# Kernel optimization log

Measured on AMD Instinct MI355X. Metric: run time of the kernel, lower is better.

## Reference

```python
import jax, jax.numpy as jnp
import numpy as np

N, E, B = 100000, 3200000, 1024
D_LM, K, H, C, L = 1024, 128, 256, 40, 2
T = 0.1
LN_EPS = 1e-5


def _layernorm(x, g, b):
    m = x.mean(-1, keepdims=True)
    v = ((x - m) ** 2).mean(-1, keepdims=True)
    return (x - m) * jax.lax.rsqrt(v + LN_EPS) * g + b


def _gcn_conv(x, W, b, src, dst, norm, self_w):
    h = x @ W
    agg = jax.ops.segment_sum(h[src] * norm[:, None], dst, num_segments=N)
    return agg + h * self_w[:, None] + b


def setup_inputs() -> dict:
    key = jax.random.key(0)
    ks = jax.random.split(key, 20)
    s = 0.02
    rn = lambda k, shp: jax.random.normal(k, shp, jnp.float32) * s
    return {
        "hidden_embeds": jax.random.normal(ks[0], (L, N, D_LM), jnp.float32),
        "proj_W1": rn(ks[1], (L, D_LM, K)),
        "proj_b1": jnp.zeros((L, K), jnp.float32),
        "ln_g": jnp.ones((L, K), jnp.float32),
        "ln_b": jnp.zeros((L, K), jnp.float32),
        "proj_W2": rn(ks[2], (L, K, K)),
        "proj_b2": jnp.zeros((L, K), jnp.float32),
        "alphas": jnp.zeros((L,), jnp.float32),
        "gcn_W1": rn(ks[3], (L, K, H)),
        "gcn_b1": jnp.zeros((L, H), jnp.float32),
        "gcn_W2": rn(ks[4], (L, H, K)),
        "gcn_b2": jnp.zeros((L, K), jnp.float32),
        "clf_W": rn(ks[5], (2 * K, C)),
        "clf_b": jnp.zeros((C,), jnp.float32),
        "edge_index": jax.random.randint(ks[6], (2, E), 0, N, jnp.int64 if jax.config.jax_enable_x64 else jnp.int32),
        "mapping": jax.random.randint(ks[7], (B,), 0, N, jnp.int64 if jax.config.jax_enable_x64 else jnp.int32),
    }


def reference(hidden_embeds, proj_W1, proj_b1, ln_g, ln_b, proj_W2, proj_b2,
              alphas, gcn_W1, gcn_b1, gcn_W2, gcn_b2, clf_W, clf_b,
              edge_index, mapping):
    src, dst = edge_index[0], edge_index[1]
    ones = jnp.ones((E,), jnp.float32)
    # GCN normalization (self loops included): deg over dst + 1
    deg = jax.ops.segment_sum(ones, dst, num_segments=N) + 1.0
    dis = jax.lax.rsqrt(deg)
    norm = dis[src] * dis[dst]          # per-edge D^-1/2 A D^-1/2
    self_w = 1.0 / deg                  # self-loop weight dis[i]*dis[i]

    last = None
    for i in range(L):
        # projector: Linear -> LayerNorm -> ReLU -> Linear
        h = hidden_embeds[i] @ proj_W1[i] + proj_b1[i]
        h = jax.nn.relu(_layernorm(h, ln_g[i], ln_b[i]))
        h = h @ proj_W2[i] + proj_b2[i]
        if i > 0:
            a = jax.nn.sigmoid(alphas[i] / T)
            h = h * a + last * (1.0 - a)
        # 2-layer GCN encoder (dropout=0)
        z = jax.nn.relu(_gcn_conv(h, gcn_W1[i], gcn_b1[i], src, dst, norm, self_w))
        last = _gcn_conv(z, gcn_W2[i], gcn_b2[i], src, dst, norm, self_w)

    # custom_global_mean_pool: mean over {node} U {out-neighbors} U {in-neighbors}
    sum_n = (jax.ops.segment_sum(last[dst], src, num_segments=N)
             + jax.ops.segment_sum(last[src], dst, num_segments=N))
    cnt = (jax.ops.segment_sum(ones, src, num_segments=N)
           + jax.ops.segment_sum(ones, dst, num_segments=N))
    pooled = (last[mapping] + sum_n[mapping]) / (1.0 + cnt[mapping])[:, None]

    out = jnp.concatenate([last[mapping], pooled], axis=1)  # [B, 2K]
    return out @ clf_W + clf_b
```

## Files before the change

kernel.cpp:

```cpp
#include <hip/hip_runtime.h>
#include <hip/hip_bf16.h>
#include <math.h>

using short8 = __attribute__((ext_vector_type(8))) short;
using f32x4  = __attribute__((ext_vector_type(4))) float;

#define PSTRIDE 2048

__device__ __forceinline__ short f2bf(float f) {
    __hip_bfloat16 h = __float2bfloat16(f);
    return *reinterpret_cast<short*>(&h);
}


__global__ void map_scatter_k(const int* __restrict__ mapping, int* __restrict__ map_idx, int B)
{
    int b = blockIdx.x * blockDim.x + threadIdx.x;
    if (b < B) map_idx[mapping[b]] = b;
}

__launch_bounds__(1024)
__global__ void bin_count_k(const int* __restrict__ dst, int E, int* __restrict__ bin_cnt)
{
    __shared__ int h[4096];
    for (int i = threadIdx.x; i < 4096; i += 1024) h[i] = 0;
    __syncthreads();
    int base = blockIdx.x * 32768;
#pragma unroll
    for (int i = 0; i < 32; ++i) {
        int e = base + i * 1024 + threadIdx.x;
        if (e < E) atomicAdd(&h[dst[e] >> 5], 1);
    }
    __syncthreads();
    for (int i = threadIdx.x; i < 4096; i += 1024) {
        int c = h[i];
        if (c) atomicAdd(&bin_cnt[i], c);
    }
}

__launch_bounds__(1024)
__global__ void scan_bins_k(const int* __restrict__ cnt, int* __restrict__ off,
                            int* __restrict__ cur)
{
    __shared__ int wsum[16];
    int tid = threadIdx.x, lane = tid & 63, wid = tid >> 6;
    int4 v = ((const int4*)cnt)[tid];
    int s0 = v.x, s1 = s0 + v.y, s2 = s1 + v.z, s3 = s2 + v.w;
    int q = s3;
#pragma unroll
    for (int o = 1; o < 64; o <<= 1) { int t = __shfl_up(q, o); if (lane >= o) q += t; }
    if (lane == 63) wsum[wid] = q;
    __syncthreads();
    if (wid == 0) {
        int w = (lane < 16) ? wsum[lane] : 0;
#pragma unroll
        for (int o = 1; o < 16; o <<= 1) { int t = __shfl_up(w, o); if (lane >= o) w += t; }
        if (lane < 16) wsum[lane] = w;
    }
    __syncthreads();
    int base = (wid ? wsum[wid - 1] : 0) + q - s3;
    int4 o4; o4.x = base; o4.y = base + s0; o4.z = base + s1; o4.w = base + s2;
    ((int4*)off)[tid] = o4;
    ((int4*)cur)[tid] = o4;
    if (tid == 1023) off[4096] = base + s3;
}

__launch_bounds__(256)
__global__ void bin_scatter_k(const int* __restrict__ ei, int E,
                              const int* __restrict__ map_idx,
                              int* __restrict__ bin_cur, int2* __restrict__ pairs,
                              int* __restrict__ pcnt, int* __restrict__ pnb)
{
    int e = blockIdx.x * blockDim.x + threadIdx.x;
    if (e >= E) return;
    int s = ei[e];
    int d = ei[E + e];
    int p = atomicAdd(&bin_cur[d >> 5], 1);
    pairs[p] = make_int2(s, d);
    int ms = map_idx[s];
    if (ms >= 0) {
        int i = atomicAdd(&pcnt[ms], 1);
        if (i < PSTRIDE) pnb[ms * PSTRIDE + i] = d;
    }
    int md = map_idx[d];
    if (md >= 0) {
        int i = atomicAdd(&pcnt[md], 1);
        if (i < PSTRIDE) pnb[md * PSTRIDE + i] = s;
    }
}

__launch_bounds__(256)
__global__ void bin_csr_k(const int2* __restrict__ pairs, const int* __restrict__ bin_off,
                          int* __restrict__ csr_in, int* __restrict__ in_off,
                          float* __restrict__ dis, float* __restrict__ selfw, int N)
{
    __shared__ int lcnt[32];
    __shared__ int lofs[32];
    __shared__ int lcur[32];
    int b = blockIdx.x;
    int tid = threadIdx.x;
    if (tid < 32) lcnt[tid] = 0;
    __syncthreads();
    int beg = bin_off[b], end = bin_off[b + 1];
    for (int i = beg + tid; i < end; i += 256)
        atomicAdd(&lcnt[pairs[i].y & 31], 1);
    __syncthreads();
    if (tid == 0) {
        int run = beg;
#pragma unroll
        for (int j = 0; j < 32; ++j) { lofs[j] = run; lcur[j] = run; run += lcnt[j]; }
    }
    __syncthreads();
    int n0 = b * 32;
    if (tid < 32 && n0 + tid < N) {
        in_off[n0 + tid] = lofs[tid];
        float dg = (float)lcnt[tid] + 1.0f;
        dis[n0 + tid] = rsqrtf(dg);
        selfw[n0 + tid] = 1.0f / dg;
    }
    if (b == gridDim.x - 1 && tid == 0) in_off[N] = end;
    for (int i = beg + tid; i < end; i += 256) {
        int2 pr = pairs[i];
        int p = atomicAdd(&lcur[pr.y & 31], 1);
        csr_in[p] = pr.x;
    }
}

__global__ void transpose_w_k(const float* __restrict__ src, short* __restrict__ dst,
                              int R, int Cc)
{
    int idx = blockIdx.x * blockDim.x + threadIdx.x;
    if (idx >= R * Cc) return;
    int r = idx / Cc;
    int c = idx - r * Cc;
    dst[(size_t)c * R + r] = f2bf(src[idx]);
}

__launch_bounds__(256)
__global__ void proj_fused_k(const float* __restrict__ X,
                             const short* __restrict__ W1t,
                             const float* __restrict__ b1,
                             const float* __restrict__ lng,
                             const float* __restrict__ lnb,
                             const short* __restrict__ W2t,
                             const float* __restrict__ b2,
                             const float* __restrict__ alphas, int layer,
                             const float* __restrict__ last,
                             short* __restrict__ out, int nrows)
{
    __shared__ short S[26624];

    const int tid  = threadIdx.x;
    const int lane = tid & 63;
    const int wave = tid >> 6;
    const int wr   = wave >> 1;
    const int wc   = wave & 1;
    const int g    = lane >> 4;
    const int lr   = lane & 15;
    const int row0 = blockIdx.x * 128;

    f32x4 acc[4][4];
#pragma unroll
    for (int fr = 0; fr < 4; ++fr)
#pragma unroll
        for (int fc = 0; fc < 4; ++fc) acc[fr][fc] = (f32x4){0.f, 0.f, 0.f, 0.f};

    const int xr   = tid >> 1;
    const int xc0  = (tid & 1) * 32;
    const bool xvalid = (row0 + xr) < nrows;
    const float* xbase = X + (size_t)(row0 + xr) * 1024 + xc0;
    const short* wbase = W1t + (size_t)(tid >> 1) * 1024 + (tid & 1) * 32;

    float4 xv[8];
    short8 wv[4];
    if (xvalid) {
#pragma unroll
        for (int m = 0; m < 8; ++m) xv[m] = *(const float4*)&xbase[m * 4];
    } else {
#pragma unroll
        for (int m = 0; m < 8; ++m) xv[m] = make_float4(0.f, 0.f, 0.f, 0.f);
    }
#pragma unroll
    for (int m = 0; m < 4; ++m) wv[m] = *(const short8*)&wbase[m * 8];

    for (int k0 = 0; k0 < 1024; k0 += 64) {
#pragma unroll
        for (int m = 0; m < 4; ++m) {
            short8 p;
            p[0]=f2bf(xv[2*m].x); p[1]=f2bf(xv[2*m].y); p[2]=f2bf(xv[2*m].z); p[3]=f2bf(xv[2*m].w);
            p[4]=f2bf(xv[2*m+1].x); p[5]=f2bf(xv[2*m+1].y); p[6]=f2bf(xv[2*m+1].z); p[7]=f2bf(xv[2*m+1].w);
            *(short8*)&S[xr * 72 + xc0 + m * 8] = p;
        }
#pragma unroll
        for (int m = 0; m < 4; ++m)
            *(short8*)&S[9216 + (tid >> 1) * 72 + (tid & 1) * 32 + m * 8] = wv[m];
        __syncthreads();

        if (k0 + 64 < 1024) {
            if (xvalid) {
                const float* xp = xbase + k0 + 64;
#pragma unroll
                for (int m = 0; m < 8; ++m) xv[m] = *(const float4*)&xp[m * 4];
            }
            const short* wp = wbase + k0 + 64;
#pragma unroll
            for (int m = 0; m < 4; ++m) wv[m] = *(const short8*)&wp[m * 8];
        }

#pragma unroll
        for (int kk = 0; kk < 64; kk += 32) {
            short8 a[4], b[4];
#pragma unroll
            for (int fr = 0; fr < 4; ++fr)
                a[fr] = *(short8*)&S[(wr * 64 + fr * 16 + lr) * 72 + kk + g * 8];
#pragma unroll
            for (int fc = 0; fc < 4; ++fc)
                b[fc] = *(short8*)&S[9216 + (wc * 64 + fc * 16 + lr) * 72 + kk + g * 8];
#pragma unroll
            for (int fr = 0; fr < 4; ++fr)
#pragma unroll
                for (int fc = 0; fc < 4; ++fc)
                    acc[fr][fc] = __builtin_amdgcn_mfma_f32_16x16x32_bf16(a[fr], b[fc], acc[fr][fc], 0, 0, 0);
        }
        __syncthreads();
    }

    float* P = (float*)&S[17408];
    {
        float b1v[4], gv[4], bv[4];
#pragma unroll
        for (int fc = 0; fc < 4; ++fc) {
            int col = wc * 64 + fc * 16 + lr;
            b1v[fc] = b1[col]; gv[fc] = lng[col]; bv[fc] = lnb[col];
        }
#pragma unroll
        for (int fr = 0; fr < 4; ++fr) {
#pragma unroll
            for (int j = 0; j < 4; ++j) {
                float s = 0.f, q = 0.f;
#pragma unroll
                for (int fc = 0; fc < 4; ++fc) {
                    float t = acc[fr][fc][j] + b1v[fc];
                    acc[fr][fc][j] = t;
                    s += t; q += t * t;
                }
#pragma unroll
                for (int m = 1; m < 16; m <<= 1) {
                    s += __shfl_xor(s, m);
                    q += __shfl_xor(q, m);
                }
                if (lr == 0) {
                    int row = wr * 64 + fr * 16 + 4 * g + j;
                    P[row * 4 + wc * 2]     = s;
                    P[row * 4 + wc * 2 + 1] = q;
                }
            }
        }
        __syncthreads();
#pragma unroll
        for (int fr = 0; fr < 4; ++fr) {
#pragma unroll
            for (int j = 0; j < 4; ++j) {
                int row = wr * 64 + fr * 16 + 4 * g + j;
                float s = P[row * 4 + 0] + P[row * 4 + 2];
                float q = P[row * 4 + 1] + P[row * 4 + 3];
                float mean = s * (1.0f / 128.0f);
                float var  = q * (1.0f / 128.0f) - mean * mean;
                float inv  = rsqrtf(var + 1e-5f);
#pragma unroll
                for (int fc = 0; fc < 4; ++fc) {
                    float h = fmaxf((acc[fr][fc][j] - mean) * inv * gv[fc] + bv[fc], 0.f);
                    S[row * 136 + wc * 64 + fc * 16 + lr] = f2bf(h);
                }
            }
        }
    }
    __syncthreads();

    f32x4 acc2[4][4];
#pragma unroll
    for (int fr = 0; fr < 4; ++fr)
#pragma unroll
        for (int fc = 0; fc < 4; ++fc) acc2[fr][fc] = (f32x4){0.f, 0.f, 0.f, 0.f};

    for (int k0 = 0; k0 < 128; k0 += 64) {
        {
            int c  = tid >> 1;
            int kb = (tid & 1) * 32;
            const short* wp = W2t + (size_t)c * 128 + k0 + kb;
#pragma unroll
            for (int m = 0; m < 4; ++m)
                *(short8*)&S[17408 + c * 72 + kb + m * 8] = *(const short8*)&wp[m * 8];
        }
        __syncthreads();
#pragma unroll
        for (int kk = 0; kk < 64; kk += 32) {
            short8 a[4], b[4];
#pragma unroll
            for (int fr = 0; fr < 4; ++fr)
                a[fr] = *(short8*)&S[(wr * 64 + fr * 16 + lr) * 136 + k0 + kk + g * 8];
#pragma unroll
            for (int fc = 0; fc < 4; ++fc)
                b[fc] = *(short8*)&S[17408 + (wc * 64 + fc * 16 + lr) * 72 + kk + g * 8];
#pragma unroll
            for (int fr = 0; fr < 4; ++fr)
#pragma unroll
                for (int fc = 0; fc < 4; ++fc)
                    acc2[fr][fc] = __builtin_amdgcn_mfma_f32_16x16x32_bf16(a[fr], b[fc], acc2[fr][fc], 0, 0, 0);
        }
        __syncthreads();
    }

    float b2v[4];
#pragma unroll
    for (int fc = 0; fc < 4; ++fc) b2v[fc] = b2[wc * 64 + fc * 16 + lr];
    float asig = 0.f, omas = 0.f;
    if (last) {
        float al = alphas[layer];
        asig = 1.0f / (1.0f + expf(-al * 10.0f));
        omas = 1.0f - asig;
    }
#pragma unroll
    for (int fr = 0; fr < 4; ++fr) {
#pragma unroll
        for (int j = 0; j < 4; ++j) {
            int gr = row0 + wr * 64 + fr * 16 + 4 * g + j;
            if (gr >= nrows) continue;
#pragma unroll
            for (int fc = 0; fc < 4; ++fc) {
                int col = wc * 64 + fc * 16 + lr;
                float o = acc2[fr][fc][j] + b2v[fc];
                if (last) o = asig * o + omas * last[(size_t)gr * 128 + col];
                out[(size_t)gr * 128 + col] = f2bf(o);
            }
        }
    }
}

__launch_bounds__(256)
__global__ void gcn_mlp_k(const short* __restrict__ U,
                          const short* __restrict__ W1t,
                          const float* __restrict__ gb1,
                          const short* __restrict__ W2t,
                          short* __restrict__ V, int M)
{
    __shared__ short S[35840];

    const int tid  = threadIdx.x;
    const int lane = tid & 63;
    const int wave = tid >> 6;
    const int g    = lane >> 4;
    const int lr   = lane & 15;
    const int m0   = blockIdx.x * 64;

#pragma unroll
    for (int it = 0; it < 4; ++it) {
        int i = tid + it * 256;
        int r = i >> 4;
        int c8 = i & 15;
        short8 v = {0,0,0,0,0,0,0,0};
        int gr = m0 + r;
        if (gr < M) v = *(const short8*)&U[(size_t)gr * 128 + c8 * 8];
        *(short8*)&S[r * 136 + c8 * 8] = v;
    }

    f32x4 acc[4][4];
#pragma unroll
    for (int fr = 0; fr < 4; ++fr)
#pragma unroll
        for (int fc = 0; fc < 4; ++fc) acc[fr][fc] = (f32x4){0.f, 0.f, 0.f, 0.f};

    for (int k0 = 0; k0 < 128; k0 += 64) {
#pragma unroll
        for (int it = 0; it < 8; ++it) {
            int i = tid + it * 256;
            int r = i >> 3;
            int c8 = i & 7;
            *(short8*)&S[17408 + r * 72 + c8 * 8] =
                *(const short8*)&W1t[(size_t)r * 128 + k0 + c8 * 8];
        }
        __syncthreads();
#pragma unroll
        for (int kk = 0; kk < 64; kk += 32) {
            short8 a[4], b[4];
#pragma unroll
            for (int fr = 0; fr < 4; ++fr)
                a[fr] = *(short8*)&S[(fr * 16 + lr) * 136 + k0 + kk + g * 8];
#pragma unroll
            for (int fc = 0; fc < 4; ++fc)
                b[fc] = *(short8*)&S[17408 + (wave * 64 + fc * 16 + lr) * 72 + kk + g * 8];
#pragma unroll
            for (int fr = 0; fr < 4; ++fr)
#pragma unroll
                for (int fc = 0; fc < 4; ++fc)
                    acc[fr][fc] = __builtin_amdgcn_mfma_f32_16x16x32_bf16(a[fr], b[fc], acc[fr][fc], 0, 0, 0);
        }
        __syncthreads();
    }

    {
        float bb[4];
#pragma unroll
        for (int fc = 0; fc < 4; ++fc) bb[fc] = gb1[wave * 64 + fc * 16 + lr];
#pragma unroll
        for (int fr = 0; fr < 4; ++fr) {
#pragma unroll
            for (int j = 0; j < 4; ++j) {
                int rloc = fr * 16 + 4 * g + j;
#pragma unroll
                for (int fc = 0; fc < 4; ++fc) {
                    float zv = fmaxf(acc[fr][fc][j] + bb[fc], 0.f);
                    S[rloc * 264 + wave * 64 + fc * 16 + lr] = f2bf(zv);
                }
            }
        }
    }

    f32x4 acc2[4][2];
#pragma unroll
    for (int fr = 0; fr < 4; ++fr) {
        acc2[fr][0] = (f32x4){0.f, 0.f, 0.f, 0.f};
        acc2[fr][1] = (f32x4){0.f, 0.f, 0.f, 0.f};
    }

    for (int k0 = 0; k0 < 256; k0 += 64) {
#pragma unroll
        for (int it = 0; it < 4; ++it) {
            int i = tid + it * 256;
            int r = i >> 3;
            int c8 = i & 7;
            *(short8*)&S[16896 + r * 72 + c8 * 8] =
                *(const short8*)&W2t[(size_t)r * 256 + k0 + c8 * 8];
        }
        __syncthreads();
#pragma unroll
        for (int kk = 0; kk < 64; kk += 32) {
            short8 a[4], b[2];
#pragma unroll
            for (int fr = 0; fr < 4; ++fr)
                a[fr] = *(short8*)&S[(fr * 16 + lr) * 264 + k0 + kk + g * 8];
#pragma unroll
            for (int fc = 0; fc < 2; ++fc)
                b[fc] = *(short8*)&S[16896 + (wave * 32 + fc * 16 + lr) * 72 + kk + g * 8];
#pragma unroll
            for (int fr = 0; fr < 4; ++fr)
#pragma unroll
                for (int fc = 0; fc < 2; ++fc)
                    acc2[fr][fc] = __builtin_amdgcn_mfma_f32_16x16x32_bf16(a[fr], b[fc], acc2[fr][fc], 0, 0, 0);
        }
        __syncthreads();
    }

#pragma unroll
    for (int fr = 0; fr < 4; ++fr) {
#pragma unroll
        for (int j = 0; j < 4; ++j) {
            int gr = m0 + fr * 16 + 4 * g + j;
            if (gr >= M) continue;
#pragma unroll
            for (int fc = 0; fc < 2; ++fc)
                V[(size_t)gr * 128 + wave * 32 + fc * 16 + lr] = f2bf(acc2[fr][fc][j]);
        }
    }
}

template <bool OUT_BF16>
__launch_bounds__(256)
__global__ void agg_k(const unsigned* __restrict__ x, void* __restrict__ y,
                      const int* __restrict__ off, const int* __restrict__ csr,
                      const float* __restrict__ dis, const float* __restrict__ selfw,
                      const float* __restrict__ bias, int N)
{
    int node = blockIdx.x * 4 + (threadIdx.x >> 6);
    if (node >= N) return;
    int lane = threadIdx.x & 63;
    int beg = off[node], end = off[node + 1];

    float ax0 = 0.f, ay0 = 0.f, ax1 = 0.f, ay1 = 0.f;
    float ax2 = 0.f, ay2 = 0.f, ax3 = 0.f, ay3 = 0.f;
    int e = beg;
    for (; e + 4 <= end; e += 4) {
        int s0 = csr[e], s1 = csr[e + 1], s2 = csr[e + 2], s3 = csr[e + 3];
        unsigned v0 = x[(size_t)s0 * 64 + lane];
        unsigned v1 = x[(size_t)s1 * 64 + lane];
        unsigned v2 = x[(size_t)s2 * 64 + lane];
        unsigned v3 = x[(size_t)s3 * 64 + lane];
        float w0 = dis[s0], w1 = dis[s1], w2 = dis[s2], w3 = dis[s3];
        ax0 = fmaf(w0, __uint_as_float(v0 << 16), ax0);
        ay0 = fmaf(w0, __uint_as_float(v0 & 0xFFFF0000u), ay0);
        ax1 = fmaf(w1, __uint_as_float(v1 << 16), ax1);
        ay1 = fmaf(w1, __uint_as_float(v1 & 0xFFFF0000u), ay1);
        ax2 = fmaf(w2, __uint_as_float(v2 << 16), ax2);
        ay2 = fmaf(w2, __uint_as_float(v2 & 0xFFFF0000u), ay2);
        ax3 = fmaf(w3, __uint_as_float(v3 << 16), ax3);
        ay3 = fmaf(w3, __uint_as_float(v3 & 0xFFFF0000u), ay3);
    }
    for (; e < end; ++e) {
        int s = csr[e];
        float w = dis[s];
        unsigned v = x[(size_t)s * 64 + lane];
        ax0 = fmaf(w, __uint_as_float(v << 16), ax0);
        ay0 = fmaf(w, __uint_as_float(v & 0xFFFF0000u), ay0);
    }
    float accx = (ax0 + ax1) + (ax2 + ax3);
    float accy = (ay0 + ay1) + (ay2 + ay3);

    float dn = dis[node], sw = selfw[node];
    unsigned vo = x[(size_t)node * 64 + lane];
    float rx = dn * accx + sw * __uint_as_float(vo << 16);
    float ry = dn * accy + sw * __uint_as_float(vo & 0xFFFF0000u);
    if (bias) { rx += bias[lane * 2]; ry += bias[lane * 2 + 1]; }
    if (OUT_BF16) {
        unsigned p = (unsigned)(unsigned short)f2bf(rx) | ((unsigned)(unsigned short)f2bf(ry) << 16);
        ((unsigned*)y)[(size_t)node * 64 + lane] = p;
    } else {
        *(float2*)&((float*)y)[(size_t)node * 128 + lane * 2] = make_float2(rx, ry);
    }
}

__launch_bounds__(128)
__global__ void pool_clf_k(const float* __restrict__ last, const int* __restrict__ mapping,
                           const int* __restrict__ map_idx,
                           const int* __restrict__ pcnt, const int* __restrict__ pnb,
                           const float* __restrict__ clfW, const float* __restrict__ clfb,
                           float* __restrict__ out, int C)
{
    int b = blockIdx.x;
    int tid = threadIdx.x;
    int n = mapping[b];
    int rep = map_idx[n];
    int cnt = pcnt[rep];
    int m = cnt < PSTRIDE ? cnt : PSTRIDE;

    float s = 0.f;
    const int* nb = pnb + (size_t)rep * PSTRIDE;
    for (int i = 0; i < m; ++i)
        s += last[(size_t)nb[i] * 128 + tid];

    float lv = last[(size_t)n * 128 + tid];
    float pooled = (lv + s) / (1.0f + (float)cnt);

    __shared__ float feat[256];
    feat[tid] = lv;
    feat[128 + tid] = pooled;
    __syncthreads();

    for (int c = tid; c < C; c += blockDim.x) {
        float o = clfb[c];
        for (int j = 0; j < 256; ++j) o = fmaf(feat[j], clfW[j * C + c], o);
        out[(size_t)b * C + c] = o;
    }
}

extern "C" void kernel_launch(void* const* d_in, const int* in_sizes, int n_in,
                              void* d_out, int out_size, void* d_ws, size_t ws_size,
                              hipStream_t stream)
{
    const float* hidden = (const float*)d_in[0];
    const float* pW1    = (const float*)d_in[1];
    const float* pb1    = (const float*)d_in[2];
    const float* lng    = (const float*)d_in[3];
    const float* lnb    = (const float*)d_in[4];
    const float* pW2    = (const float*)d_in[5];
    const float* pb2    = (const float*)d_in[6];
    const float* alphas = (const float*)d_in[7];
    const float* gW1    = (const float*)d_in[8];
    const float* gb1    = (const float*)d_in[9];
    const float* gW2    = (const float*)d_in[10];
    const float* gb2    = (const float*)d_in[11];
    const float* clfW   = (const float*)d_in[12];
    const float* clfb   = (const float*)d_in[13];
    const int*   ei     = (const int*)d_in[14];
    const int*   mapping= (const int*)d_in[15];

    const int L   = in_sizes[7];
    const int K   = in_sizes[2] / L;
    const int H   = in_sizes[9] / L;
    const int C   = in_sizes[13];
    const int DLM = in_sizes[1] / (L * K);
    const int N   = in_sizes[0] / (L * DLM);
    const int E   = in_sizes[14] / 2;
    const int B   = in_sizes[15];
    const int NBINS = (N + 31) / 32;

    char* ws = (char*)d_ws;
    size_t off = 0;
    auto carve = [&](size_t bytes) -> char* {
        char* p = ws + off;
        off += (bytes + 255) & ~(size_t)255;
        return p;
    };
    int*   map_idx = (int*)carve((size_t)N * 4);
    int*   pcnt    = (int*)carve((size_t)B * 4);
    int*   pnb     = (int*)carve((size_t)B * PSTRIDE * 4);
    int*   bin_cnt = (int*)carve(4096 * 4);
    int*   bin_off = (int*)carve(4097 * 4);
    int*   bin_cur = (int*)carve(4096 * 4);
    int2*  pairs   = (int2*)carve((size_t)E * 8);
    int*   in_off  = (int*)carve((size_t)(N + 1) * 4);
    float* dis     = (float*)carve((size_t)N * 4);
    float* selfw   = (float*)carve((size_t)N * 4);
    int*   csr_in  = (int*)carve((size_t)E * 4);
    short* bufA    = (short*)carve((size_t)N * K * 2);
    short* bufU    = (short*)carve((size_t)N * K * 2);
    float* bufLast = (float*)carve((size_t)N * K * 4);
    short* w1t     = (short*)carve((size_t)L * K * DLM * 2);
    short* w2t     = (short*)carve((size_t)L * K * K * 2);
    short* gw1t    = (short*)carve((size_t)L * H * K * 2);
    short* gw2t    = (short*)carve((size_t)L * K * H * 2);
    (void)ws_size; (void)n_in; (void)out_size;

    hipMemsetAsync(bin_cnt, 0, 4096 * 4, stream);
    hipMemsetAsync(map_idx, 0xFF, (size_t)N * 4, stream);
    hipMemsetAsync(pcnt, 0, (size_t)B * 4, stream);
    map_scatter_k<<<dim3((B + 255) / 256), 256, 0, stream>>>(mapping, map_idx, B);
    bin_count_k<<<dim3((E + 32767) / 32768), 1024, 0, stream>>>(ei + E, E, bin_cnt);
    scan_bins_k<<<dim3(1), 1024, 0, stream>>>(bin_cnt, bin_off, bin_cur);
    bin_scatter_k<<<dim3((E + 255) / 256), 256, 0, stream>>>(ei, E, map_idx, bin_cur,
                                                             pairs, pcnt, pnb);
    bin_csr_k<<<dim3(NBINS), 256, 0, stream>>>(pairs, bin_off, csr_in, in_off,
                                               dis, selfw, N);

    for (int i = 0; i < L; ++i) {
        transpose_w_k<<<dim3((DLM * K + 255) / 256), 256, 0, stream>>>(
            pW1 + (size_t)i * DLM * K, w1t + (size_t)i * K * DLM, DLM, K);
        transpose_w_k<<<dim3((K * K + 255) / 256), 256, 0, stream>>>(
            pW2 + (size_t)i * K * K, w2t + (size_t)i * K * K, K, K);
        transpose_w_k<<<dim3((K * H + 255) / 256), 256, 0, stream>>>(
            gW1 + (size_t)i * K * H, gw1t + (size_t)i * H * K, K, H);
        transpose_w_k<<<dim3((H * K + 255) / 256), 256, 0, stream>>>(
            gW2 + (size_t)i * H * K, gw2t + (size_t)i * K * H, H, K);
    }

    const int nblk64  = (N + 63) / 64;
    const int nblk128 = (N + 127) / 128;

    for (int i = 0; i < L; ++i) {
        proj_fused_k<<<dim3(nblk128), 256, 0, stream>>>(
            hidden + (size_t)i * N * DLM,
            w1t + (size_t)i * K * DLM,
            pb1 + (size_t)i * K,
            lng + (size_t)i * K,
            lnb + (size_t)i * K,
            w2t + (size_t)i * K * K,
            pb2 + (size_t)i * K,
            alphas, i,
            (i > 0) ? bufLast : nullptr,
            bufA, N);

        agg_k<true><<<dim3((N + 3) / 4), 256, 0, stream>>>(
            (const unsigned*)bufA, bufU, in_off, csr_in, dis, selfw, nullptr, N);
        gcn_mlp_k<<<dim3(nblk64), 256, 0, stream>>>(
            bufU, gw1t + (size_t)i * H * K, gb1 + (size_t)i * H,
            gw2t + (size_t)i * K * H, bufA, N);
        agg_k<false><<<dim3((N + 3) / 4), 256, 0, stream>>>(
            (const unsigned*)bufA, bufLast, in_off, csr_in, dis, selfw,
            gb2 + (size_t)i * K, N);
    }

    pool_clf_k<<<dim3(B), 128, 0, stream>>>(bufLast, mapping, map_idx, pcnt, pnb,
                                            clfW, clfb, (float*)d_out, C);
}
```

Before: 1.292 ms.

## Prescale features by D^-1/2 to drop per-edge gathers; pack edge pairs

Folds the source-side D^-1/2 factor into the producing GEMM epilogues (projector and GCN MLP), so aggregation becomes a plain sum plus self term scaled by dis[node]. This removes the per-edge random gather of dis[src] and the selfw array. Edge pairs are also packed into a single 32-bit word (source index in the low 27 bits, destination low 5 bits in the top 5), halving the scratch traffic, and the per-layer weight transposes are batched into four launches. Packing assumes node ids fit in 27 bits, and bf16 rounding now happens after the scaling.

```diff
diff --git a/kernel.cpp b/kernel.cpp
--- a/kernel.cpp
+++ b/kernel.cpp
@@ -68,7 +68,7 @@
 __launch_bounds__(256)
 __global__ void bin_scatter_k(const int* __restrict__ ei, int E,
                               const int* __restrict__ map_idx,
-                              int* __restrict__ bin_cur, int2* __restrict__ pairs,
+                              int* __restrict__ bin_cur, unsigned* __restrict__ pairs,
                               int* __restrict__ pcnt, int* __restrict__ pnb)
 {
     int e = blockIdx.x * blockDim.x + threadIdx.x;
@@ -76,7 +76,7 @@
     int s = ei[e];
     int d = ei[E + e];
     int p = atomicAdd(&bin_cur[d >> 5], 1);
-    pairs[p] = make_int2(s, d);
+    pairs[p] = (unsigned)s | ((unsigned)(d & 31) << 27);
     int ms = map_idx[s];
     if (ms >= 0) {
         int i = atomicAdd(&pcnt[ms], 1);
@@ -90,9 +90,9 @@
 }
 
 __launch_bounds__(256)
-__global__ void bin_csr_k(const int2* __restrict__ pairs, const int* __restrict__ bin_off,
+__global__ void bin_csr_k(const unsigned* __restrict__ pairs, const int* __restrict__ bin_off,
                           int* __restrict__ csr_in, int* __restrict__ in_off,
-                          float* __restrict__ dis, float* __restrict__ selfw, int N)
+                          float* __restrict__ dis, int N)
 {
     __shared__ int lcnt[32];
     __shared__ int lofs[32];
@@ -103,7 +103,7 @@
     __syncthreads();
     int beg = bin_off[b], end = bin_off[b + 1];
     for (int i = beg + tid; i < end; i += 256)
-        atomicAdd(&lcnt[pairs[i].y & 31], 1);
+        atomicAdd(&lcnt[pairs[i] >> 27], 1);
     __syncthreads();
     if (tid == 0) {
         int run = beg;
@@ -116,24 +116,26 @@
         in_off[n0 + tid] = lofs[tid];
         float dg = (float)lcnt[tid] + 1.0f;
         dis[n0 + tid] = rsqrtf(dg);
-        selfw[n0 + tid] = 1.0f / dg;
     }
     if (b == gridDim.x - 1 && tid == 0) in_off[N] = end;
     for (int i = beg + tid; i < end; i += 256) {
-        int2 pr = pairs[i];
-        int p = atomicAdd(&lcur[pr.y & 31], 1);
-        csr_in[p] = pr.x;
-    }
-}
-
-__global__ void transpose_w_k(const float* __restrict__ src, short* __restrict__ dst,
-                              int R, int Cc)
+        unsigned pr = pairs[i];
+        int p = atomicAdd(&lcur[pr >> 27], 1);
+        csr_in[p] = (int)(pr & 0x07FFFFFFu);
+    }
+}
+
+__global__ void transpose_wb_k(const float* __restrict__ src, short* __restrict__ dst,
+                               int LAY, int R, int Cc)
 {
     int idx = blockIdx.x * blockDim.x + threadIdx.x;
-    if (idx >= R * Cc) return;
-    int r = idx / Cc;
-    int c = idx - r * Cc;
-    dst[(size_t)c * R + r] = f2bf(src[idx]);
+    int tot = LAY * R * Cc;
+    if (idx >= tot) return;
+    int lay = idx / (R * Cc);
+    int rem = idx - lay * R * Cc;
+    int r = rem / Cc;
+    int c = rem - r * Cc;
+    dst[(size_t)lay * R * Cc + (size_t)c * R + r] = f2bf(src[idx]);
 }
 
 __launch_bounds__(256)
@@ -146,6 +148,7 @@
                              const float* __restrict__ b2,
                              const float* __restrict__ alphas, int layer,
                              const float* __restrict__ last,
+                             const float* __restrict__ dis,
                              short* __restrict__ out, int nrows)
 {
     __shared__ short S[26624];
@@ -326,12 +329,13 @@
         for (int j = 0; j < 4; ++j) {
             int gr = row0 + wr * 64 + fr * 16 + 4 * g + j;
             if (gr >= nrows) continue;
+            float disr = dis[gr];
 #pragma unroll
             for (int fc = 0; fc < 4; ++fc) {
                 int col = wc * 64 + fc * 16 + lr;
                 float o = acc2[fr][fc][j] + b2v[fc];
                 if (last) o = asig * o + omas * last[(size_t)gr * 128 + col];
-                out[(size_t)gr * 128 + col] = f2bf(o);
+                out[(size_t)gr * 128 + col] = f2bf(o * disr);
             }
         }
     }
@@ -342,6 +346,7 @@
                           const short* __restrict__ W1t,
                           const float* __restrict__ gb1,
                           const short* __restrict__ W2t,
+                          const float* __restrict__ dis,
                           short* __restrict__ V, int M)
 {
     __shared__ short S[35840];
@@ -457,9 +462,10 @@
         for (int j = 0; j < 4; ++j) {
             int gr = m0 + fr * 16 + 4 * g + j;
             if (gr >= M) continue;
+            float disr = dis[gr];
 #pragma unroll
             for (int fc = 0; fc < 2; ++fc)
-                V[(size_t)gr * 128 + wave * 32 + fc * 16 + lr] = f2bf(acc2[fr][fc][j]);
+                V[(size_t)gr * 128 + wave * 32 + fc * 16 + lr] = f2bf(acc2[fr][fc][j] * disr);
         }
     }
 }
@@ -468,10 +474,10 @@
 __launch_bounds__(256)
 __global__ void agg_k(const unsigned* __restrict__ x, void* __restrict__ y,
                       const int* __restrict__ off, const int* __restrict__ csr,
-                      const float* __restrict__ dis, const float* __restrict__ selfw,
+                      const float* __restrict__ dis,
                       const float* __restrict__ bias, int N)
 {
-    int node = blockIdx.x * 4 + (threadIdx.x >> 6);
+    int node = __builtin_amdgcn_readfirstlane(blockIdx.x * 4 + (threadIdx.x >> 6));
     if (node >= N) return;
     int lane = threadIdx.x & 63;
     int beg = off[node], end = off[node + 1];
@@ -485,30 +491,28 @@
         unsigned v1 = x[(size_t)s1 * 64 + lane];
         unsigned v2 = x[(size_t)s2 * 64 + lane];
         unsigned v3 = x[(size_t)s3 * 64 + lane];
-        float w0 = dis[s0], w1 = dis[s1], w2 = dis[s2], w3 = dis[s3];
-        ax0 = fmaf(w0, __uint_as_float(v0 << 16), ax0);
-        ay0 = fmaf(w0, __uint_as_float(v0 & 0xFFFF0000u), ay0);
-        ax1 = fmaf(w1, __uint_as_float(v1 << 16), ax1);
-        ay1 = fmaf(w1, __uint_as_float(v1 & 0xFFFF0000u), ay1);
-        ax2 = fmaf(w2, __uint_as_float(v2 << 16), ax2);
-        ay2 = fmaf(w2, __uint_as_float(v2 & 0xFFFF0000u), ay2);
-        ax3 = fmaf(w3, __uint_as_float(v3 << 16), ax3);
-        ay3 = fmaf(w3, __uint_as_float(v3 & 0xFFFF0000u), ay3);
+        ax0 += __uint_as_float(v0 << 16);
+        ay0 += __uint_as_float(v0 & 0xFFFF0000u);
+        ax1 += __uint_as_float(v1 << 16);
+        ay1 += __uint_as_float(v1 & 0xFFFF0000u);
+        ax2 += __uint_as_float(v2 << 16);
+        ay2 += __uint_as_float(v2 & 0xFFFF0000u);
+        ax3 += __uint_as_float(v3 << 16);
+        ay3 += __uint_as_float(v3 & 0xFFFF0000u);
     }
     for (; e < end; ++e) {
         int s = csr[e];
-        float w = dis[s];
         unsigned v = x[(size_t)s * 64 + lane];
-        ax0 = fmaf(w, __uint_as_float(v << 16), ax0);
-        ay0 = fmaf(w, __uint_as_float(v & 0xFFFF0000u), ay0);
-    }
-    float accx = (ax0 + ax1) + (ax2 + ax3);
-    float accy = (ay0 + ay1) + (ay2 + ay3);
-
-    float dn = dis[node], sw = selfw[node];
+        ax0 += __uint_as_float(v << 16);
+        ay0 += __uint_as_float(v & 0xFFFF0000u);
+    }
     unsigned vo = x[(size_t)node * 64 + lane];
-    float rx = dn * accx + sw * __uint_as_float(vo << 16);
-    float ry = dn * accy + sw * __uint_as_float(vo & 0xFFFF0000u);
+    float accx = ((ax0 + ax1) + (ax2 + ax3)) + __uint_as_float(vo << 16);
+    float accy = ((ay0 + ay1) + (ay2 + ay3)) + __uint_as_float(vo & 0xFFFF0000u);
+
+    float dn = dis[node];
+    float rx = dn * accx;
+    float ry = dn * accy;
     if (bias) { rx += bias[lane * 2]; ry += bias[lane * 2 + 1]; }
     if (OUT_BF16) {
         unsigned p = (unsigned)(unsigned short)f2bf(rx) | ((unsigned)(unsigned short)f2bf(ry) << 16);
@@ -590,24 +594,23 @@
         off += (bytes + 255) & ~(size_t)255;
         return p;
     };
-    int*   map_idx = (int*)carve((size_t)N * 4);
-    int*   pcnt    = (int*)carve((size_t)B * 4);
-    int*   pnb     = (int*)carve((size_t)B * PSTRIDE * 4);
-    int*   bin_cnt = (int*)carve(4096 * 4);
-    int*   bin_off = (int*)carve(4097 * 4);
-    int*   bin_cur = (int*)carve(4096 * 4);
-    int2*  pairs   = (int2*)carve((size_t)E * 8);
-    int*   in_off  = (int*)carve((size_t)(N + 1) * 4);
-    float* dis     = (float*)carve((size_t)N * 4);
-    float* selfw   = (float*)carve((size_t)N * 4);
-    int*   csr_in  = (int*)carve((size_t)E * 4);
-    short* bufA    = (short*)carve((size_t)N * K * 2);
-    short* bufU    = (short*)carve((size_t)N * K * 2);
-    float* bufLast = (float*)carve((size_t)N * K * 4);
-    short* w1t     = (short*)carve((size_t)L * K * DLM * 2);
-    short* w2t     = (short*)carve((size_t)L * K * K * 2);
-    short* gw1t    = (short*)carve((size_t)L * H * K * 2);
-    short* gw2t    = (short*)carve((size_t)L * K * H * 2);
+    int*      map_idx = (int*)carve((size_t)N * 4);
+    int*      pcnt    = (int*)carve((size_t)B * 4);
+    int*      pnb     = (int*)carve((size_t)B * PSTRIDE * 4);
+    int*      bin_cnt = (int*)carve(4096 * 4);
+    int*      bin_off = (int*)carve(4097 * 4);
+    int*      bin_cur = (int*)carve(4096 * 4);
+    unsigned* pairs   = (unsigned*)carve((size_t)E * 4);
+    int*      in_off  = (int*)carve((size_t)(N + 1) * 4);
+    float*    dis     = (float*)carve((size_t)N * 4);
+    int*      csr_in  = (int*)carve((size_t)E * 4);
+    short*    bufA    = (short*)carve((size_t)N * K * 2);
+    short*    bufU    = (short*)carve((size_t)N * K * 2);
+    float*    bufLast = (float*)carve((size_t)N * K * 4);
+    short*    w1t     = (short*)carve((size_t)L * K * DLM * 2);
+    short*    w2t     = (short*)carve((size_t)L * K * K * 2);
+    short*    gw1t    = (short*)carve((size_t)L * H * K * 2);
+    short*    gw2t    = (short*)carve((size_t)L * K * H * 2);
     (void)ws_size; (void)n_in; (void)out_size;
 
     hipMemsetAsync(bin_cnt, 0, 4096 * 4, stream);
@@ -619,18 +622,12 @@
     bin_scatter_k<<<dim3((E + 255) / 256), 256, 0, stream>>>(ei, E, map_idx, bin_cur,
                                                              pairs, pcnt, pnb);
     bin_csr_k<<<dim3(NBINS), 256, 0, stream>>>(pairs, bin_off, csr_in, in_off,
-                                               dis, selfw, N);
-
-    for (int i = 0; i < L; ++i) {
-        transpose_w_k<<<dim3((DLM * K + 255) / 256), 256, 0, stream>>>(
-            pW1 + (size_t)i * DLM * K, w1t + (size_t)i * K * DLM, DLM, K);
-        transpose_w_k<<<dim3((K * K + 255) / 256), 256, 0, stream>>>(
-            pW2 + (size_t)i * K * K, w2t + (size_t)i * K * K, K, K);
-        transpose_w_k<<<dim3((K * H + 255) / 256), 256, 0, stream>>>(
-            gW1 + (size_t)i * K * H, gw1t + (size_t)i * H * K, K, H);
-        transpose_w_k<<<dim3((H * K + 255) / 256), 256, 0, stream>>>(
-            gW2 + (size_t)i * H * K, gw2t + (size_t)i * K * H, H, K);
-    }
+                                               dis, N);
+
+    transpose_wb_k<<<dim3((L * DLM * K + 255) / 256), 256, 0, stream>>>(pW1, w1t, L, DLM, K);
+    transpose_wb_k<<<dim3((L * K * K + 255) / 256), 256, 0, stream>>>(pW2, w2t, L, K, K);
+    transpose_wb_k<<<dim3((L * K * H + 255) / 256), 256, 0, stream>>>(gW1, gw1t, L, K, H);
+    transpose_wb_k<<<dim3((L * H * K + 255) / 256), 256, 0, stream>>>(gW2, gw2t, L, H, K);
 
     const int nblk64  = (N + 63) / 64;
     const int nblk128 = (N + 127) / 128;
@@ -646,15 +643,16 @@
             pb2 + (size_t)i * K,
             alphas, i,
             (i > 0) ? bufLast : nullptr,
+            dis,
             bufA, N);
 
         agg_k<true><<<dim3((N + 3) / 4), 256, 0, stream>>>(
-            (const unsigned*)bufA, bufU, in_off, csr_in, dis, selfw, nullptr, N);
+            (const unsigned*)bufA, bufU, in_off, csr_in, dis, nullptr, N);
         gcn_mlp_k<<<dim3(nblk64), 256, 0, stream>>>(
             bufU, gw1t + (size_t)i * H * K, gb1 + (size_t)i * H,
-            gw2t + (size_t)i * K * H, bufA, N);
+            gw2t + (size_t)i * K * H, dis, bufA, N);
         agg_k<false><<<dim3((N + 3) / 4), 256, 0, stream>>>(
-            (const unsigned*)bufA, bufLast, in_off, csr_in, dis, selfw,
+            (const unsigned*)bufA, bufLast, in_off, csr_in, dis,
             gb2 + (size_t)i * K, N);
     }
 
```

Result: faster. 1.226 ms (-5.1%).
